# Performance work log

Hardware: AMD Instinct MI355X
Metric: run time of the kernel (lower is better)

The kernel has to match this reference:

```python
import jax, jax.numpy as jnp
import numpy as np

B, S, D, H = 4, 2048, 1024, 16
DK = D // H  # 64


def setup_inputs() -> dict:
    key = jax.random.key(0)
    ks = jax.random.split(key, 9)
    x = jax.random.normal(ks[0], (B, S, D), dtype=jnp.float32)
    # causal mask, broadcast over batch and heads
    attn_mask = jnp.tril(jnp.ones((S, S), dtype=jnp.int32))[None, None]
    scale = 0.02
    Wq = jax.random.normal(ks[1], (D, D), dtype=jnp.float32) * scale
    Wk = jax.random.normal(ks[2], (D, D), dtype=jnp.float32) * scale
    Wv = jax.random.normal(ks[3], (D, D), dtype=jnp.float32) * scale
    Wo = jax.random.normal(ks[4], (D, D), dtype=jnp.float32) * scale
    bq = jax.random.normal(ks[5], (D,), dtype=jnp.float32) * scale
    bk = jax.random.normal(ks[6], (D,), dtype=jnp.float32) * scale
    bv = jax.random.normal(ks[7], (D,), dtype=jnp.float32) * scale
    bo = jax.random.normal(ks[8], (D,), dtype=jnp.float32) * scale
    return {"x": x, "attn_mask": attn_mask, "Wq": Wq, "bq": bq, "Wk": Wk,
            "bk": bk, "Wv": Wv, "bv": bv, "Wo": Wo, "bo": bo}


def reference(x, attn_mask, Wq, bq, Wk, bk, Wv, bv, Wo, bo):
    b, s, d = x.shape
    # projections -> [b, h, s, dk]
    def proj(W, bias):
        return (x @ W + bias).reshape(b, s, H, DK).transpose(0, 2, 1, 3)
    q = proj(Wq, bq)
    k = proj(Wk, bk)
    v = proj(Wv, bv)
    # scores [b, h, s, s]
    scores = jnp.einsum('bhqd,bhkd->bhqk', q, k) / jnp.sqrt(jnp.float32(DK))
    scores = jnp.where(attn_mask == 0, jnp.float32(-1e9), scores)
    probs = jax.nn.softmax(scores, axis=-1)  # dropout_rate=0 -> identity
    attn_out = jnp.einsum('bhqk,bhkd->bhqd', probs, v)
    # combine heads -> [b, s, d], then output projection
    attn_out = attn_out.transpose(0, 2, 1, 3).reshape(b, s, d)
    return attn_out @ Wo + bo
```

## Files before the change

kernel.cpp:

```cpp
#include <hip/hip_runtime.h>
#include <hip/hip_bf16.h>
#include <stdint.h>

#define S_LEN 2048
#define DMODEL 1024
#define NH 16
#define DK 64
#define BATCH 4
#define KDIM 1024
#define SCQ 0.18033688f

using bf16 = __hip_bfloat16;
using bf162 = __hip_bfloat162;

typedef __bf16 v_bf16x8 __attribute__((ext_vector_type(8)));
typedef short v_s16x4 __attribute__((ext_vector_type(4)));
typedef float v_f32x4 __attribute__((ext_vector_type(4)));

union PackB4 { v_s16x4 v; bf162 h[2]; };

struct alignas(8) BF4 { bf16 a, b, c, d; };

__global__ __launch_bounds__(256) void cvt_f32_bf16(const float* __restrict__ in,
                                                    bf16* __restrict__ out) {
    size_t i = ((size_t)blockIdx.x * 256 + threadIdx.x) * 4;
    float4 v = *(const float4*)(in + i);
    BF4 r;
    r.a = __float2bfloat16(v.x);
    r.b = __float2bfloat16(v.y);
    r.c = __float2bfloat16(v.z);
    r.d = __float2bfloat16(v.w);
    *(BF4*)(out + i) = r;
}

__global__ __launch_bounds__(256) void transpose_cvt4(
    const float* __restrict__ W0, const float* __restrict__ W1,
    const float* __restrict__ W2, const float* __restrict__ W3,
    bf16* __restrict__ Wt4) {
    __shared__ float tile[32][33];
    const int z = blockIdx.z;
    const float* W = (z == 0) ? W0 : (z == 1) ? W1 : (z == 2) ? W2 : W3;
    bf16* Wt = Wt4 + (size_t)z * DMODEL * DMODEL;
    const float sc = (z == 0) ? SCQ : 1.0f;
    int tx = threadIdx.x, ty = threadIdx.y;
    int k0 = blockIdx.x * 32, n0 = blockIdx.y * 32;
    #pragma unroll
    for (int i = 0; i < 4; i++) {
        int k = k0 + ty + 8 * i;
        tile[ty + 8 * i][tx] = W[(size_t)k * DMODEL + n0 + tx];
    }
    __syncthreads();
    #pragma unroll
    for (int i = 0; i < 4; i++) {
        int n = n0 + ty + 8 * i;
        Wt[(size_t)n * DMODEL + k0 + tx] = __float2bfloat16(tile[tx][ty + 8 * i] * sc);
    }
}

__global__ __launch_bounds__(256) void gemm_qkv(
    const bf16* __restrict__ A, const bf16* __restrict__ Wt4,
    const float* __restrict__ bq, const float* __restrict__ bk,
    const float* __restrict__ bv,
    bf16* __restrict__ Qo, bf16* __restrict__ Ko, bf16* __restrict__ Vto)
{
    __shared__ __align__(16) short As[128 * 32];
    __shared__ __align__(16) short Bs[128 * 32];
    const int z = blockIdx.z;
    const bf16* Bt = Wt4 + (size_t)z * DMODEL * DMODEL;
    const float* bias = (z == 0) ? bq : (z == 1) ? bk : bv;
    const float bsc = (z == 0) ? SCQ : 1.0f;

    const int t = threadIdx.x;
    const int lane = t & 63;
    const int wave = t >> 6;
    const int quad = lane >> 4;
    const int l15 = lane & 15;
    const int m0 = blockIdx.x * 128;
    const int n0 = blockIdx.y * 128;
    const int wRow = (wave >> 1) * 64;
    const int wCol = (wave & 1) * 64;

    const int r0 = t >> 2, p0 = t & 3;
    const int r1 = (t + 256) >> 2, p1 = (t + 256) & 3;

    const short* ArowBase = (z == 2) ? Bs : As;
    const short* BrowBase = (z == 2) ? As : Bs;

    v_f32x4 acc[4][4] = {};

    for (int k0 = 0; k0 < KDIM; k0 += 32) {
        uint4 a0 = *(const uint4*)(A + (size_t)(m0 + r0) * KDIM + k0 + p0 * 8);
        uint4 a1 = *(const uint4*)(A + (size_t)(m0 + r1) * KDIM + k0 + p1 * 8);
        uint4 b0 = *(const uint4*)(Bt + (size_t)(n0 + r0) * KDIM + k0 + p0 * 8);
        uint4 b1 = *(const uint4*)(Bt + (size_t)(n0 + r1) * KDIM + k0 + p1 * 8);
        __syncthreads();
        *(uint4*)(As + r0 * 32 + p0 * 8) = a0;
        *(uint4*)(As + r1 * 32 + p1 * 8) = a1;
        *(uint4*)(Bs + r0 * 32 + p0 * 8) = b0;
        *(uint4*)(Bs + r1 * 32 + p1 * 8) = b1;
        __syncthreads();

        v_bf16x8 af[4], bfr[4];
        #pragma unroll
        for (int mt = 0; mt < 4; mt++) {
            int r = wRow + mt * 16 + l15;
            af[mt] = *(const v_bf16x8*)(ArowBase + r * 32 + quad * 8);
        }
        #pragma unroll
        for (int nt = 0; nt < 4; nt++) {
            int r = wCol + nt * 16 + l15;
            bfr[nt] = *(const v_bf16x8*)(BrowBase + r * 32 + quad * 8);
        }
        #pragma unroll
        for (int mt = 0; mt < 4; mt++)
            #pragma unroll
            for (int nt = 0; nt < 4; nt++)
                acc[mt][nt] = __builtin_amdgcn_mfma_f32_16x16x32_bf16(
                    af[mt], bfr[nt], acc[mt][nt], 0, 0, 0);
    }

    if (z != 2) {
        bf16* C = (z == 0) ? Qo : Ko;
        float bvv[4];
        #pragma unroll
        for (int nt = 0; nt < 4; nt++)
            bvv[nt] = bias[n0 + wCol + nt * 16 + l15] * bsc;
        #pragma unroll
        for (int mt = 0; mt < 4; mt++)
            #pragma unroll
            for (int nt = 0; nt < 4; nt++)
                #pragma unroll
                for (int r = 0; r < 4; r++) {
                    int row = m0 + wRow + mt * 16 + quad * 4 + r;
                    int col = n0 + wCol + nt * 16 + l15;
                    int b = row >> 11, s = row & (S_LEN - 1);
                    int h = col >> 6, dk = col & (DK - 1);
                    C[(((size_t)(b * NH + h)) * S_LEN + s) * DK + dk] =
                        __float2bfloat16(acc[mt][nt][r] + bvv[nt]);
                }
    } else {
        float bvv[4][4];
        #pragma unroll
        for (int mt = 0; mt < 4; mt++)
            #pragma unroll
            for (int r = 0; r < 4; r++)
                bvv[mt][r] = bias[n0 + wRow + mt * 16 + quad * 4 + r];
        #pragma unroll
        for (int mt = 0; mt < 4; mt++)
            #pragma unroll
            for (int nt = 0; nt < 4; nt++)
                #pragma unroll
                for (int r = 0; r < 4; r++) {
                    int ng = n0 + wRow + mt * 16 + quad * 4 + r;
                    int rowg = m0 + wCol + nt * 16 + l15;
                    int b = rowg >> 11, s = rowg & (S_LEN - 1);
                    int h = ng >> 6, dk = ng & (DK - 1);
                    Vto[(((size_t)(b * NH + h)) * DK + dk) * S_LEN + s] =
                        __float2bfloat16(acc[mt][nt][r] + bvv[mt][r]);
                }
    }
}

__global__ __launch_bounds__(256) void gemm_o(
    const bf16* __restrict__ A, const bf16* __restrict__ Bt,
    const float* __restrict__ bias, float* __restrict__ C)
{
    __shared__ __align__(16) short As[128 * 32];
    __shared__ __align__(16) short Bs[128 * 32];
    const int t = threadIdx.x;
    const int lane = t & 63;
    const int wave = t >> 6;
    const int quad = lane >> 4;
    const int l15 = lane & 15;
    const int m0 = blockIdx.x * 128;
    const int n0 = blockIdx.y * 128;
    const int wRow = (wave >> 1) * 64;
    const int wCol = (wave & 1) * 64;

    const int r0 = t >> 2, p0 = t & 3;
    const int r1 = (t + 256) >> 2, p1 = (t + 256) & 3;

    v_f32x4 acc[4][4] = {};

    for (int k0 = 0; k0 < KDIM; k0 += 32) {
        uint4 a0 = *(const uint4*)(A + (size_t)(m0 + r0) * KDIM + k0 + p0 * 8);
        uint4 a1 = *(const uint4*)(A + (size_t)(m0 + r1) * KDIM + k0 + p1 * 8);
        uint4 b0 = *(const uint4*)(Bt + (size_t)(n0 + r0) * KDIM + k0 + p0 * 8);
        uint4 b1 = *(const uint4*)(Bt + (size_t)(n0 + r1) * KDIM + k0 + p1 * 8);
        __syncthreads();
        *(uint4*)(As + r0 * 32 + p0 * 8) = a0;
        *(uint4*)(As + r1 * 32 + p1 * 8) = a1;
        *(uint4*)(Bs + r0 * 32 + p0 * 8) = b0;
        *(uint4*)(Bs + r1 * 32 + p1 * 8) = b1;
        __syncthreads();

        v_bf16x8 af[4], bfr[4];
        #pragma unroll
        for (int mt = 0; mt < 4; mt++) {
            int r = wRow + mt * 16 + l15;
            af[mt] = *(const v_bf16x8*)(As + r * 32 + quad * 8);
        }
        #pragma unroll
        for (int nt = 0; nt < 4; nt++) {
            int r = wCol + nt * 16 + l15;
            bfr[nt] = *(const v_bf16x8*)(Bs + r * 32 + quad * 8);
        }
        #pragma unroll
        for (int mt = 0; mt < 4; mt++)
            #pragma unroll
            for (int nt = 0; nt < 4; nt++)
                acc[mt][nt] = __builtin_amdgcn_mfma_f32_16x16x32_bf16(
                    af[mt], bfr[nt], acc[mt][nt], 0, 0, 0);
    }

    float bvv[4];
    #pragma unroll
    for (int nt = 0; nt < 4; nt++) bvv[nt] = bias[n0 + wCol + nt * 16 + l15];

    #pragma unroll
    for (int mt = 0; mt < 4; mt++)
        #pragma unroll
        for (int nt = 0; nt < 4; nt++)
            #pragma unroll
            for (int r = 0; r < 4; r++) {
                int row = m0 + wRow + mt * 16 + quad * 4 + r;
                int col = n0 + wCol + nt * 16 + l15;
                C[(size_t)row * DMODEL + col] = acc[mt][nt][r] + bvv[nt];
            }
}

__global__ __launch_bounds__(256) void attn_mfma(
    const bf16* __restrict__ Qg, const bf16* __restrict__ Kg,
    const bf16* __restrict__ Vtg, bf16* __restrict__ Og)
{
    __shared__ __align__(16) short lds[16896];
    short* Ks = lds;
    short* Vs = lds + 8192;

    const int t = threadIdx.x;
    const int lane = t & 63;
    const int wave = t >> 6;
    const int quad = lane >> 4;
    const int l15 = lane & 15;
    const int bh = blockIdx.x;
    const int yy = (gridDim.y - 1) - blockIdx.y;
    const int q0 = yy * 128;

    const size_t baseK = (size_t)bh * S_LEN * DK;
    const size_t baseVt = (size_t)bh * DK * S_LEN;

    v_bf16x8 qf[2][2];
    #pragma unroll
    for (int qt = 0; qt < 2; qt++) {
        int q = q0 + wave * 32 + qt * 16 + l15;
        #pragma unroll
        for (int kc = 0; kc < 2; kc++)
            qf[qt][kc] = *(const v_bf16x8*)(Qg + baseK + (size_t)q * DK + kc * 32 + quad * 8);
    }

    v_f32x4 oacc[2][4] = {};
    float mrun[2] = {-1e30f, -1e30f};
    float lrun[2] = {0.f, 0.f};

    for (int tt = 0; tt <= yy; tt++) {
        int k0 = tt * 128;
        __syncthreads();
        #pragma unroll
        for (int i = 0; i < 4; i++) {
            int c = t + 256 * i;
            int r = c >> 3, p = c & 7;
            uint4 val = *(const uint4*)(Kg + baseK + (size_t)(k0 + r) * DK + p * 8);
            *(uint4*)(Ks + r * 64 + (p ^ (r & 7)) * 8) = val;
        }
        #pragma unroll
        for (int i = 0; i < 4; i++) {
            int c = t + 256 * i;
            int d = c >> 4, p = c & 15;
            uint4 val = *(const uint4*)(Vtg + baseVt + (size_t)d * S_LEN + k0 + p * 8);
            *(uint4*)(Vs + d * 136 + p * 8) = val;
        }
        __syncthreads();

        v_f32x4 s_[8][2];
        #pragma unroll
        for (int kt = 0; kt < 8; kt++) {
            int krow = kt * 16 + l15;
            v_bf16x8 kf0 = *(const v_bf16x8*)(Ks + krow * 64 + ((quad) ^ (krow & 7)) * 8);
            v_bf16x8 kf1 = *(const v_bf16x8*)(Ks + krow * 64 + ((4 + quad) ^ (krow & 7)) * 8);
            #pragma unroll
            for (int qt = 0; qt < 2; qt++) {
                v_f32x4 a = {};
                a = __builtin_amdgcn_mfma_f32_16x16x32_bf16(kf0, qf[qt][0], a, 0, 0, 0);
                a = __builtin_amdgcn_mfma_f32_16x16x32_bf16(kf1, qf[qt][1], a, 0, 0, 0);
                s_[kt][qt] = a;
            }
        }

        if (tt == yy) {
            #pragma unroll
            for (int kt = 0; kt < 8; kt++)
                #pragma unroll
                for (int qt = 0; qt < 2; qt++) {
                    int qq = wave * 32 + qt * 16 + l15;
                    #pragma unroll
                    for (int r = 0; r < 4; r++) {
                        int key = kt * 16 + quad * 4 + r;
                        if (key > qq) s_[kt][qt][r] = -1e30f;
                    }
                }
        }

        float tmax[2] = {-1e30f, -1e30f};
        #pragma unroll
        for (int kt = 0; kt < 8; kt++)
            #pragma unroll
            for (int qt = 0; qt < 2; qt++)
                #pragma unroll
                for (int r = 0; r < 4; r++)
                    tmax[qt] = fmaxf(tmax[qt], s_[kt][qt][r]);
        #pragma unroll
        for (int qt = 0; qt < 2; qt++) {
            tmax[qt] = fmaxf(tmax[qt], __shfl_xor(tmax[qt], 16));
            tmax[qt] = fmaxf(tmax[qt], __shfl_xor(tmax[qt], 32));
        }
        float alpha[2];
        #pragma unroll
        for (int qt = 0; qt < 2; qt++) {
            float mn = fmaxf(mrun[qt], tmax[qt]);
            alpha[qt] = __builtin_amdgcn_exp2f(mrun[qt] - mn);
            mrun[qt] = mn;
        }
        float lsum[2] = {0.f, 0.f};
        #pragma unroll
        for (int kt = 0; kt < 8; kt++)
            #pragma unroll
            for (int qt = 0; qt < 2; qt++)
                #pragma unroll
                for (int r = 0; r < 4; r++) {
                    float p = __builtin_amdgcn_exp2f(s_[kt][qt][r] - mrun[qt]);
                    s_[kt][qt][r] = p;
                    lsum[qt] += p;
                }
        #pragma unroll
        for (int qt = 0; qt < 2; qt++) {
            lsum[qt] += __shfl_xor(lsum[qt], 16);
            lsum[qt] += __shfl_xor(lsum[qt], 32);
            lrun[qt] = lrun[qt] * alpha[qt] + lsum[qt];
        }
        #pragma unroll
        for (int qt = 0; qt < 2; qt++)
            #pragma unroll
            for (int dt = 0; dt < 4; dt++)
                #pragma unroll
                for (int r = 0; r < 4; r++)
                    oacc[qt][dt][r] *= alpha[qt];

        #pragma unroll
        for (int kt = 0; kt < 8; kt++) {
            v_s16x4 vf[4];
            #pragma unroll
            for (int dt = 0; dt < 4; dt++)
                vf[dt] = *(const v_s16x4*)(Vs + (dt * 16 + l15) * 136 + kt * 16 + quad * 4);
            #pragma unroll
            for (int qt = 0; qt < 2; qt++) {
                PackB4 pu;
                pu.h[0] = __float22bfloat162_rn(make_float2(s_[kt][qt][0], s_[kt][qt][1]));
                pu.h[1] = __float22bfloat162_rn(make_float2(s_[kt][qt][2], s_[kt][qt][3]));
                #pragma unroll
                for (int dt = 0; dt < 4; dt++)
                    oacc[qt][dt] = __builtin_amdgcn_mfma_f32_16x16x16bf16_1k(
                        vf[dt], pu.v, oacc[qt][dt], 0, 0, 0);
            }
        }
    }

    __syncthreads();
    #pragma unroll
    for (int qt = 0; qt < 2; qt++) {
        float inv = 1.f / lrun[qt];
        int qloc = wave * 32 + qt * 16 + l15;
        #pragma unroll
        for (int dt = 0; dt < 4; dt++) {
            PackB4 ou;
            ou.h[0] = __float22bfloat162_rn(
                make_float2(oacc[qt][dt][0] * inv, oacc[qt][dt][1] * inv));
            ou.h[1] = __float22bfloat162_rn(
                make_float2(oacc[qt][dt][2] * inv, oacc[qt][dt][3] * inv));
            *(v_s16x4*)(lds + qloc * 72 + dt * 16 + quad * 4) = ou.v;
        }
    }
    __syncthreads();
    {
        const int b = bh >> 4, h = bh & 15;
        int row = t >> 1, half = t & 1;
        size_t gbase = (((size_t)b * S_LEN + q0 + row) * NH + h) * DK + half * 32;
        #pragma unroll
        for (int j = 0; j < 4; j++)
            *(uint4*)(Og + gbase + j * 8) =
                *(const uint4*)(lds + row * 72 + half * 32 + j * 8);
    }
}

extern "C" void kernel_launch(void* const* d_in, const int* in_sizes, int n_in,
                              void* d_out, int out_size, void* d_ws, size_t ws_size,
                              hipStream_t stream) {
    const float* x  = (const float*)d_in[0];
    const float* Wq = (const float*)d_in[2];
    const float* bq = (const float*)d_in[3];
    const float* Wk = (const float*)d_in[4];
    const float* bk = (const float*)d_in[5];
    const float* Wv = (const float*)d_in[6];
    const float* bv = (const float*)d_in[7];
    const float* Wo = (const float*)d_in[8];
    const float* bo = (const float*)d_in[9];
    float* out = (float*)d_out;

    const size_t TEN = (size_t)BATCH * S_LEN * DMODEL * sizeof(bf16);
    char* ws = (char*)d_ws;
    bf16* xb  = (bf16*)ws;
    bf16* Vt  = (bf16*)(ws + TEN);
    bf16* Wt4 = (bf16*)(ws + 2 * TEN);
    bf16* Q   = (bf16*)d_out;
    bf16* Kt  = (bf16*)((char*)d_out + TEN);
    bf16* AO  = xb;

    hipLaunchKernelGGL(cvt_f32_bf16, dim3(BATCH * S_LEN * DMODEL / 1024), dim3(256),
                       0, stream, x, xb);

    hipLaunchKernelGGL(transpose_cvt4, dim3(DMODEL / 32, DMODEL / 32, 4), dim3(32, 8),
                       0, stream, Wq, Wk, Wv, Wo, Wt4);

    hipLaunchKernelGGL(gemm_qkv, dim3(BATCH * S_LEN / 128, DMODEL / 128, 3), dim3(256),
                       0, stream, xb, Wt4, bq, bk, bv, Q, Kt, Vt);

    hipLaunchKernelGGL(attn_mfma, dim3(BATCH * NH, S_LEN / 128), dim3(256),
                       0, stream, Q, Kt, Vt, AO);

    hipLaunchKernelGGL(gemm_o, dim3(BATCH * S_LEN / 128, DMODEL / 128), dim3(256),
                       0, stream, AO, Wt4 + (size_t)3 * DMODEL * DMODEL, bo, out);
}
```

Before: 303.8 us.

## Prefetch next K/V tile into registers and use direct global-to-LDS loads in GEMMs

The attention kernel now loads the next K/V tile into registers while the current tile's MFMA work runs, then writes it to LDS after compute, so global latency is hidden behind math. The GEMM kernels replace register-staged LDS fills with global_load_lds direct transfers. The attention kernel also gets an occupancy hint in its launch bounds and converts probabilities to bf16 right at exponentiation. The prefetch adds register pressure, which may reduce occupancy or cause spills.

```diff
diff --git a/kernel.cpp b/kernel.cpp
--- a/kernel.cpp
+++ b/kernel.cpp
@@ -18,6 +18,12 @@
 typedef float v_f32x4 __attribute__((ext_vector_type(4)));
 
 union PackB4 { v_s16x4 v; bf162 h[2]; };
+
+__device__ __forceinline__ void gll16(const void* g, void* l) {
+    __builtin_amdgcn_global_load_lds(
+        (__attribute__((address_space(1))) unsigned int*)g,
+        (__attribute__((address_space(3))) unsigned int*)l, 16, 0, 0);
+}
 
 struct alignas(8) BF4 { bf16 a, b, c, d; };
 
@@ -89,15 +95,11 @@
     v_f32x4 acc[4][4] = {};
 
     for (int k0 = 0; k0 < KDIM; k0 += 32) {
-        uint4 a0 = *(const uint4*)(A + (size_t)(m0 + r0) * KDIM + k0 + p0 * 8);
-        uint4 a1 = *(const uint4*)(A + (size_t)(m0 + r1) * KDIM + k0 + p1 * 8);
-        uint4 b0 = *(const uint4*)(Bt + (size_t)(n0 + r0) * KDIM + k0 + p0 * 8);
-        uint4 b1 = *(const uint4*)(Bt + (size_t)(n0 + r1) * KDIM + k0 + p1 * 8);
         __syncthreads();
-        *(uint4*)(As + r0 * 32 + p0 * 8) = a0;
-        *(uint4*)(As + r1 * 32 + p1 * 8) = a1;
-        *(uint4*)(Bs + r0 * 32 + p0 * 8) = b0;
-        *(uint4*)(Bs + r1 * 32 + p1 * 8) = b1;
+        gll16(A  + (size_t)(m0 + r0) * KDIM + k0 + p0 * 8, As + (size_t)t * 8);
+        gll16(A  + (size_t)(m0 + r1) * KDIM + k0 + p1 * 8, As + (size_t)t * 8 + 2048);
+        gll16(Bt + (size_t)(n0 + r0) * KDIM + k0 + p0 * 8, Bs + (size_t)t * 8);
+        gll16(Bt + (size_t)(n0 + r1) * KDIM + k0 + p1 * 8, Bs + (size_t)t * 8 + 2048);
         __syncthreads();
 
         v_bf16x8 af[4], bfr[4];
@@ -183,15 +185,11 @@
     v_f32x4 acc[4][4] = {};
 
     for (int k0 = 0; k0 < KDIM; k0 += 32) {
-        uint4 a0 = *(const uint4*)(A + (size_t)(m0 + r0) * KDIM + k0 + p0 * 8);
-        uint4 a1 = *(const uint4*)(A + (size_t)(m0 + r1) * KDIM + k0 + p1 * 8);
-        uint4 b0 = *(const uint4*)(Bt + (size_t)(n0 + r0) * KDIM + k0 + p0 * 8);
-        uint4 b1 = *(const uint4*)(Bt + (size_t)(n0 + r1) * KDIM + k0 + p1 * 8);
         __syncthreads();
-        *(uint4*)(As + r0 * 32 + p0 * 8) = a0;
-        *(uint4*)(As + r1 * 32 + p1 * 8) = a1;
-        *(uint4*)(Bs + r0 * 32 + p0 * 8) = b0;
-        *(uint4*)(Bs + r1 * 32 + p1 * 8) = b1;
+        gll16(A  + (size_t)(m0 + r0) * KDIM + k0 + p0 * 8, As + (size_t)t * 8);
+        gll16(A  + (size_t)(m0 + r1) * KDIM + k0 + p1 * 8, As + (size_t)t * 8 + 2048);
+        gll16(Bt + (size_t)(n0 + r0) * KDIM + k0 + p0 * 8, Bs + (size_t)t * 8);
+        gll16(Bt + (size_t)(n0 + r1) * KDIM + k0 + p1 * 8, Bs + (size_t)t * 8 + 2048);
         __syncthreads();
 
         v_bf16x8 af[4], bfr[4];
@@ -229,7 +227,7 @@
             }
 }
 
-__global__ __launch_bounds__(256) void attn_mfma(
+__global__ __launch_bounds__(256, 3) void attn_mfma(
     const bf16* __restrict__ Qg, const bf16* __restrict__ Kg,
     const bf16* __restrict__ Vtg, bf16* __restrict__ Og)
 {
@@ -262,24 +260,50 @@
     float mrun[2] = {-1e30f, -1e30f};
     float lrun[2] = {0.f, 0.f};
 
+    uint4 kreg[4], vreg[4];
+    #pragma unroll
+    for (int i = 0; i < 4; i++) {
+        int c = t + 256 * i;
+        int r = c >> 3, p = c & 7;
+        kreg[i] = *(const uint4*)(Kg + baseK + (size_t)r * DK + p * 8);
+    }
+    #pragma unroll
+    for (int i = 0; i < 4; i++) {
+        int c = t + 256 * i;
+        int d = c >> 4, p = c & 15;
+        vreg[i] = *(const uint4*)(Vtg + baseVt + (size_t)d * S_LEN + p * 8);
+    }
+    #pragma unroll
+    for (int i = 0; i < 4; i++) {
+        int c = t + 256 * i;
+        int r = c >> 3, p = c & 7;
+        *(uint4*)(Ks + r * 64 + (p ^ (r & 7)) * 8) = kreg[i];
+    }
+    #pragma unroll
+    for (int i = 0; i < 4; i++) {
+        int c = t + 256 * i;
+        int d = c >> 4, p = c & 15;
+        *(uint4*)(Vs + d * 136 + p * 8) = vreg[i];
+    }
+    __syncthreads();
+
     for (int tt = 0; tt <= yy; tt++) {
-        int k0 = tt * 128;
-        __syncthreads();
-        #pragma unroll
-        for (int i = 0; i < 4; i++) {
-            int c = t + 256 * i;
-            int r = c >> 3, p = c & 7;
-            uint4 val = *(const uint4*)(Kg + baseK + (size_t)(k0 + r) * DK + p * 8);
-            *(uint4*)(Ks + r * 64 + (p ^ (r & 7)) * 8) = val;
-        }
-        #pragma unroll
-        for (int i = 0; i < 4; i++) {
-            int c = t + 256 * i;
-            int d = c >> 4, p = c & 15;
-            uint4 val = *(const uint4*)(Vtg + baseVt + (size_t)d * S_LEN + k0 + p * 8);
-            *(uint4*)(Vs + d * 136 + p * 8) = val;
-        }
-        __syncthreads();
+        const bool pf = (tt < yy);
+        if (pf) {
+            int k0n = (tt + 1) * 128;
+            #pragma unroll
+            for (int i = 0; i < 4; i++) {
+                int c = t + 256 * i;
+                int r = c >> 3, p = c & 7;
+                kreg[i] = *(const uint4*)(Kg + baseK + (size_t)(k0n + r) * DK + p * 8);
+            }
+            #pragma unroll
+            for (int i = 0; i < 4; i++) {
+                int c = t + 256 * i;
+                int d = c >> 4, p = c & 15;
+                vreg[i] = *(const uint4*)(Vtg + baseVt + (size_t)d * S_LEN + k0n + p * 8);
+            }
+        }
 
         v_f32x4 s_[8][2];
         #pragma unroll
@@ -330,17 +354,21 @@
             alpha[qt] = __builtin_amdgcn_exp2f(mrun[qt] - mn);
             mrun[qt] = mn;
         }
+
         float lsum[2] = {0.f, 0.f};
+        PackB4 pk[8][2];
         #pragma unroll
         for (int kt = 0; kt < 8; kt++)
             #pragma unroll
-            for (int qt = 0; qt < 2; qt++)
-                #pragma unroll
-                for (int r = 0; r < 4; r++) {
-                    float p = __builtin_amdgcn_exp2f(s_[kt][qt][r] - mrun[qt]);
-                    s_[kt][qt][r] = p;
-                    lsum[qt] += p;
-                }
+            for (int qt = 0; qt < 2; qt++) {
+                float p0 = __builtin_amdgcn_exp2f(s_[kt][qt][0] - mrun[qt]);
+                float p1 = __builtin_amdgcn_exp2f(s_[kt][qt][1] - mrun[qt]);
+                float p2 = __builtin_amdgcn_exp2f(s_[kt][qt][2] - mrun[qt]);
+                float p3 = __builtin_amdgcn_exp2f(s_[kt][qt][3] - mrun[qt]);
+                lsum[qt] += (p0 + p1) + (p2 + p3);
+                pk[kt][qt].h[0] = __float22bfloat162_rn(make_float2(p0, p1));
+                pk[kt][qt].h[1] = __float22bfloat162_rn(make_float2(p2, p3));
+            }
         #pragma unroll
         for (int qt = 0; qt < 2; qt++) {
             lsum[qt] += __shfl_xor(lsum[qt], 16);
@@ -362,15 +390,28 @@
             for (int dt = 0; dt < 4; dt++)
                 vf[dt] = *(const v_s16x4*)(Vs + (dt * 16 + l15) * 136 + kt * 16 + quad * 4);
             #pragma unroll
-            for (int qt = 0; qt < 2; qt++) {
-                PackB4 pu;
-                pu.h[0] = __float22bfloat162_rn(make_float2(s_[kt][qt][0], s_[kt][qt][1]));
-                pu.h[1] = __float22bfloat162_rn(make_float2(s_[kt][qt][2], s_[kt][qt][3]));
+            for (int qt = 0; qt < 2; qt++)
                 #pragma unroll
                 for (int dt = 0; dt < 4; dt++)
                     oacc[qt][dt] = __builtin_amdgcn_mfma_f32_16x16x16bf16_1k(
-                        vf[dt], pu.v, oacc[qt][dt], 0, 0, 0);
-            }
+                        vf[dt], pk[kt][qt].v, oacc[qt][dt], 0, 0, 0);
+        }
+
+        if (pf) {
+            __syncthreads();
+            #pragma unroll
+            for (int i = 0; i < 4; i++) {
+                int c = t + 256 * i;
+                int r = c >> 3, p = c & 7;
+                *(uint4*)(Ks + r * 64 + (p ^ (r & 7)) * 8) = kreg[i];
+            }
+            #pragma unroll
+            for (int i = 0; i < 4; i++) {
+                int c = t + 256 * i;
+                int d = c >> 4, p = c & 15;
+                *(uint4*)(Vs + d * 136 + p * 8) = vreg[i];
+            }
+            __syncthreads();
         }
     }
 
```

After: 317.8 us. +4.6%, slower.

## Double-buffer attention K/V tiles with direct global-to-LDS loads

Applied to the files above, without the earlier changes.

The GEMM and attention tile loads now use global_load_lds, which writes global memory straight into LDS and skips the register round trip. The bank-conflict swizzle moves from the LDS store to the global source address. In attention, K/V tiles are double-buffered across two 32 KB halves, so the next tile's load is issued before computing on the current one, and only one barrier per iteration remains. The V layout changes from padded to XOR-swizzled, and s_setprio raises wave priority around the MFMA sections. The cost is 64 KB of LDS per attention block, which can lower occupancy, and correctness relies on the compiler inserting the right vmcnt waits before the barrier.

```diff
diff --git a/kernel.cpp b/kernel.cpp
--- a/kernel.cpp
+++ b/kernel.cpp
@@ -18,6 +18,12 @@
 typedef float v_f32x4 __attribute__((ext_vector_type(4)));
 
 union PackB4 { v_s16x4 v; bf162 h[2]; };
+
+__device__ __forceinline__ void gll16(const void* g, void* l) {
+    __builtin_amdgcn_global_load_lds(
+        (__attribute__((address_space(1))) unsigned int*)g,
+        (__attribute__((address_space(3))) unsigned int*)l, 16, 0, 0);
+}
 
 struct alignas(8) BF4 { bf16 a, b, c, d; };
 
@@ -89,15 +95,11 @@
     v_f32x4 acc[4][4] = {};
 
     for (int k0 = 0; k0 < KDIM; k0 += 32) {
-        uint4 a0 = *(const uint4*)(A + (size_t)(m0 + r0) * KDIM + k0 + p0 * 8);
-        uint4 a1 = *(const uint4*)(A + (size_t)(m0 + r1) * KDIM + k0 + p1 * 8);
-        uint4 b0 = *(const uint4*)(Bt + (size_t)(n0 + r0) * KDIM + k0 + p0 * 8);
-        uint4 b1 = *(const uint4*)(Bt + (size_t)(n0 + r1) * KDIM + k0 + p1 * 8);
         __syncthreads();
-        *(uint4*)(As + r0 * 32 + p0 * 8) = a0;
-        *(uint4*)(As + r1 * 32 + p1 * 8) = a1;
-        *(uint4*)(Bs + r0 * 32 + p0 * 8) = b0;
-        *(uint4*)(Bs + r1 * 32 + p1 * 8) = b1;
+        gll16(A  + (size_t)(m0 + r0) * KDIM + k0 + p0 * 8, As + (size_t)t * 8);
+        gll16(A  + (size_t)(m0 + r1) * KDIM + k0 + p1 * 8, As + (size_t)t * 8 + 2048);
+        gll16(Bt + (size_t)(n0 + r0) * KDIM + k0 + p0 * 8, Bs + (size_t)t * 8);
+        gll16(Bt + (size_t)(n0 + r1) * KDIM + k0 + p1 * 8, Bs + (size_t)t * 8 + 2048);
         __syncthreads();
 
         v_bf16x8 af[4], bfr[4];
@@ -183,15 +185,11 @@
     v_f32x4 acc[4][4] = {};
 
     for (int k0 = 0; k0 < KDIM; k0 += 32) {
-        uint4 a0 = *(const uint4*)(A + (size_t)(m0 + r0) * KDIM + k0 + p0 * 8);
-        uint4 a1 = *(const uint4*)(A + (size_t)(m0 + r1) * KDIM + k0 + p1 * 8);
-        uint4 b0 = *(const uint4*)(Bt + (size_t)(n0 + r0) * KDIM + k0 + p0 * 8);
-        uint4 b1 = *(const uint4*)(Bt + (size_t)(n0 + r1) * KDIM + k0 + p1 * 8);
         __syncthreads();
-        *(uint4*)(As + r0 * 32 + p0 * 8) = a0;
-        *(uint4*)(As + r1 * 32 + p1 * 8) = a1;
-        *(uint4*)(Bs + r0 * 32 + p0 * 8) = b0;
-        *(uint4*)(Bs + r1 * 32 + p1 * 8) = b1;
+        gll16(A  + (size_t)(m0 + r0) * KDIM + k0 + p0 * 8, As + (size_t)t * 8);
+        gll16(A  + (size_t)(m0 + r1) * KDIM + k0 + p1 * 8, As + (size_t)t * 8 + 2048);
+        gll16(Bt + (size_t)(n0 + r0) * KDIM + k0 + p0 * 8, Bs + (size_t)t * 8);
+        gll16(Bt + (size_t)(n0 + r1) * KDIM + k0 + p1 * 8, Bs + (size_t)t * 8 + 2048);
         __syncthreads();
 
         v_bf16x8 af[4], bfr[4];
@@ -233,9 +231,7 @@
     const bf16* __restrict__ Qg, const bf16* __restrict__ Kg,
     const bf16* __restrict__ Vtg, bf16* __restrict__ Og)
 {
-    __shared__ __align__(16) short lds[16896];
-    short* Ks = lds;
-    short* Vs = lds + 8192;
+    __shared__ __align__(16) short lds[32768];
 
     const int t = threadIdx.x;
     const int lane = t & 63;
@@ -249,6 +245,17 @@
     const size_t baseK = (size_t)bh * S_LEN * DK;
     const size_t baseVt = (size_t)bh * DK * S_LEN;
 
+    const bf16* srcK[4];
+    const bf16* srcV[4];
+    #pragma unroll
+    for (int i = 0; i < 4; i++) {
+        int c = t + 256 * i;
+        int rK = c >> 3, pK = (c & 7) ^ (rK & 7);
+        srcK[i] = Kg + baseK + (size_t)rK * DK + pK * 8;
+        int rV = c >> 4, pV = (c & 15) ^ (rV & 15);
+        srcV[i] = Vtg + baseVt + (size_t)rV * S_LEN + pV * 8;
+    }
+
     v_bf16x8 qf[2][2];
     #pragma unroll
     for (int qt = 0; qt < 2; qt++) {
@@ -262,26 +269,29 @@
     float mrun[2] = {-1e30f, -1e30f};
     float lrun[2] = {0.f, 0.f};
 
+    #pragma unroll
+    for (int i = 0; i < 4; i++) gll16(srcK[i], lds + (t + 256 * i) * 8);
+    #pragma unroll
+    for (int i = 0; i < 4; i++) gll16(srcV[i], lds + 8192 + (t + 256 * i) * 8);
+    __syncthreads();
+
+    int cur = 0;
     for (int tt = 0; tt <= yy; tt++) {
-        int k0 = tt * 128;
-        __syncthreads();
-        #pragma unroll
-        for (int i = 0; i < 4; i++) {
-            int c = t + 256 * i;
-            int r = c >> 3, p = c & 7;
-            uint4 val = *(const uint4*)(Kg + baseK + (size_t)(k0 + r) * DK + p * 8);
-            *(uint4*)(Ks + r * 64 + (p ^ (r & 7)) * 8) = val;
-        }
-        #pragma unroll
-        for (int i = 0; i < 4; i++) {
-            int c = t + 256 * i;
-            int d = c >> 4, p = c & 15;
-            uint4 val = *(const uint4*)(Vtg + baseVt + (size_t)d * S_LEN + k0 + p * 8);
-            *(uint4*)(Vs + d * 136 + p * 8) = val;
-        }
-        __syncthreads();
+        if (tt < yy) {
+            short* Kd = lds + ((cur ^ 1) << 14);
+            short* Vd = Kd + 8192;
+            size_t offK = (size_t)(tt + 1) * (128 * DK);
+            size_t offV = (size_t)(tt + 1) * 128;
+            #pragma unroll
+            for (int i = 0; i < 4; i++) gll16(srcK[i] + offK, Kd + (t + 256 * i) * 8);
+            #pragma unroll
+            for (int i = 0; i < 4; i++) gll16(srcV[i] + offV, Vd + (t + 256 * i) * 8);
+        }
+        const short* Ks = lds + (cur << 14);
+        const short* Vs = Ks + 8192;
 
         v_f32x4 s_[8][2];
+        __builtin_amdgcn_s_setprio(1);
         #pragma unroll
         for (int kt = 0; kt < 8; kt++) {
             int krow = kt * 16 + l15;
@@ -295,6 +305,7 @@
                 s_[kt][qt] = a;
             }
         }
+        __builtin_amdgcn_s_setprio(0);
 
         if (tt == yy) {
             #pragma unroll
@@ -355,12 +366,16 @@
                 for (int r = 0; r < 4; r++)
                     oacc[qt][dt][r] *= alpha[qt];
 
+        __builtin_amdgcn_s_setprio(1);
         #pragma unroll
         for (int kt = 0; kt < 8; kt++) {
             v_s16x4 vf[4];
             #pragma unroll
-            for (int dt = 0; dt < 4; dt++)
-                vf[dt] = *(const v_s16x4*)(Vs + (dt * 16 + l15) * 136 + kt * 16 + quad * 4);
+            for (int dt = 0; dt < 4; dt++) {
+                int q = kt * 2 + (quad >> 1);
+                vf[dt] = *(const v_s16x4*)(Vs + (dt * 16 + l15) * 128 +
+                                           ((q ^ l15) * 8 + (quad & 1) * 4));
+            }
             #pragma unroll
             for (int qt = 0; qt < 2; qt++) {
                 PackB4 pu;
@@ -372,9 +387,12 @@
                         vf[dt], pu.v, oacc[qt][dt], 0, 0, 0);
             }
         }
-    }
-
-    __syncthreads();
+        __builtin_amdgcn_s_setprio(0);
+
+        __syncthreads();
+        cur ^= 1;
+    }
+
     #pragma unroll
     for (int qt = 0; qt < 2; qt++) {
         float inv = 1.f / lrun[qt];
```

New measurement: 306.9 us. About the same (+1.0%).
